# Kernel optimization log

Measured on AMD Instinct MI355X. Metric: run time of the kernel, lower is better.

Reference implementation:

```python
import jax, jax.numpy as jnp
import numpy as np

NUM_NODES = 1_000_000
MEM_DIM = 128
MSG_DIM = 128
B = 262_144


def setup_inputs() -> dict:
    key = jax.random.key(0)
    k1, k2, k3, k4, k5, k6, k7 = jax.random.split(key, 7)
    s = 1.0 / np.sqrt(MEM_DIM)
    return {
        "memory": jax.random.normal(k1, (NUM_NODES, MEM_DIM), jnp.float32) * 0.1,
        "last_update": jnp.zeros((NUM_NODES,), jnp.float32),
        "messages": jax.random.normal(k2, (B, MSG_DIM), jnp.float32),
        "timestamps": jax.random.uniform(k3, (B,), jnp.float32),
        "W_ih": jax.random.uniform(k4, (3 * MEM_DIM, MSG_DIM), jnp.float32, -s, s),
        "W_hh": jax.random.uniform(k5, (3 * MEM_DIM, MEM_DIM), jnp.float32, -s, s),
        "b_ih": jax.random.uniform(k6, (3 * MEM_DIM,), jnp.float32, -s, s),
        "b_hh": jax.random.uniform(k7, (3 * MEM_DIM,), jnp.float32, -s, s),
        "node_ids": jax.random.randint(jax.random.fold_in(key, 99), (B,), 0, NUM_NODES, jnp.int64 if jax.config.jax_enable_x64 else jnp.int32),
    }


def gru_cell(x, h, W_ih, W_hh, b_ih, b_hh):
    # torch.nn.GRUCell math
    gi = x @ W_ih.T + b_ih  # [B, 3H]
    gh = h @ W_hh.T + b_hh  # [B, 3H]
    i_r, i_z, i_n = jnp.split(gi, 3, axis=-1)
    h_r, h_z, h_n = jnp.split(gh, 3, axis=-1)
    r = jax.nn.sigmoid(i_r + h_r)
    z = jax.nn.sigmoid(i_z + h_z)
    n = jnp.tanh(i_n + r * h_n)
    return (1.0 - z) * n + z * h


def reference(memory, last_update, messages, timestamps, W_ih, W_hh, b_ih, b_hh, node_ids):
    # gather node memory rows
    h = memory[node_ids]  # [B, MEM_DIM]
    h_new = gru_cell(messages, h, W_ih, W_hh, b_ih, b_hh)
    # scatter updated state and timestamps back into persistent buffers
    memory_new = memory.at[node_ids].set(h_new)
    last_update_new = last_update.at[node_ids].set(timestamps)
    return memory_new, last_update_new
```

## Files before the change

kernel.cpp:

```cpp
#include <hip/hip_runtime.h>
#include <stdint.h>

#define NN   1000000
#define DD   128
#define BT   262144
#define TR   32
#define NT   8
#define RPB  (TR * NT)
#define GRID_GRU (BT / RPB)

typedef __attribute__((ext_vector_type(8))) short bf16x8;
typedef __attribute__((ext_vector_type(4))) float f32x4;

__device__ __forceinline__ unsigned short f2bf(float f) {
    union { float f; uint32_t u; } c; c.f = f;
    uint32_t u = c.u + 0x7FFFu + ((c.u >> 16) & 1u);
    return (unsigned short)(u >> 16);
}
__device__ __forceinline__ float bf2f(unsigned short s) {
    union { uint32_t u; float f; } c; c.u = ((uint32_t)s) << 16;
    return c.f;
}
__device__ __forceinline__ float sigmoid_f(float x) {
    return 1.0f / (1.0f + __expf(-x));
}
__device__ __forceinline__ float tanh_f(float x) {
    return 2.0f / (1.0f + __expf(-2.0f * x)) - 1.0f;
}
__device__ __forceinline__ bf16x8 cvt8(float4 a, float4 b) {
    bf16x8 v;
    v[0] = (short)f2bf(a.x); v[1] = (short)f2bf(a.y);
    v[2] = (short)f2bf(a.z); v[3] = (short)f2bf(a.w);
    v[4] = (short)f2bf(b.x); v[5] = (short)f2bf(b.y);
    v[6] = (short)f2bf(b.z); v[7] = (short)f2bf(b.w);
    return v;
}

__global__ __launch_bounds__(256) void k_winner(const int* __restrict__ node_ids,
                                                int* __restrict__ winner) {
    int i = blockIdx.x * 256 + threadIdx.x;
    if (i < BT) atomicMax(&winner[node_ids[i]], i);
}

__global__ __launch_bounds__(256) void k_copy(const float4* __restrict__ mem_in,
                                              const float* __restrict__ lu_in,
                                              const float* __restrict__ ts,
                                              const int* __restrict__ winner,
                                              float4* __restrict__ mem_out,
                                              float* __restrict__ lu_out) {
    const long NV4 = (long)NN * 32;
    const long TOTAL = NV4 + NN;
    long stride = (long)gridDim.x * 256;
    for (long i = blockIdx.x * 256L + threadIdx.x; i < TOTAL; i += stride) {
        if (i < NV4) {
            int node = (int)(i >> 5);
            if (winner[node] < 0) mem_out[i] = mem_in[i];
        } else {
            int v = (int)(i - NV4);
            int w = winner[v];
            lu_out[v] = (w >= 0) ? ts[w] : lu_in[v];
        }
    }
}

__global__ __launch_bounds__(512, 2) void k_gru(const float* __restrict__ memory,
                                                const float* __restrict__ messages,
                                                const float* __restrict__ W_ih,
                                                const float* __restrict__ W_hh,
                                                const float* __restrict__ b_ih,
                                                const float* __restrict__ b_hh,
                                                const int* __restrict__ node_ids,
                                                const int* __restrict__ winner,
                                                float* __restrict__ out_mem) {
    __shared__ unsigned short x_lds[2][TR * DD];
    __shared__ unsigned short h_lds[2][TR * DD];
    __shared__ int s_nid[RPB];
    __shared__ unsigned char s_win[RPB];

    const int tid = threadIdx.x;
    const int rowBase = blockIdx.x * RPB;

    for (int i = tid; i < RPB; i += 512) {
        int brow = rowBase + i;
        int nid = node_ids[brow];
        s_nid[i] = nid;
        s_win[i] = (winner[nid] == brow) ? 1 : 0;
    }
    __syncthreads();

    const int lane  = tid & 63;
    const int wave  = tid >> 6;
    const int l15   = lane & 15;
    const int khalf = lane >> 4;
    const int jcol  = wave * 16 + l15;

    bf16x8 wf[6][4];
#pragma unroll
    for (int g = 0; g < 3; ++g) {
#pragma unroll
        for (int ks = 0; ks < 4; ++ks) {
            const float* p = W_ih + (size_t)(g * 128 + jcol) * DD + ks * 32 + khalf * 8;
            wf[g][ks] = cvt8(*(const float4*)p, *(const float4*)(p + 4));
            const float* q = W_hh + (size_t)(g * 128 + jcol) * DD + ks * 32 + khalf * 8;
            wf[3 + g][ks] = cvt8(*(const float4*)q, *(const float4*)(q + 4));
        }
    }
    const float bir = b_ih[jcol], biz = b_ih[128 + jcol], bin = b_ih[256 + jcol];
    const float bhr = b_hh[jcol], bhz = b_hh[128 + jcol], bhn = b_hh[256 + jcol];

    const int sr  = tid >> 4;
    const int sc8 = (tid & 15) * 8;
    const int ldsOff = sr * 256 + ((sc8 * 2) ^ ((sr & 7) << 4));

    float4 px0, px1, ph0, ph1;
    {
        const float* xp = messages + (size_t)(rowBase + sr) * DD + sc8;
        px0 = ((const float4*)xp)[0]; px1 = ((const float4*)xp)[1];
        const float* hp = memory + (size_t)s_nid[sr] * DD + sc8;
        ph0 = ((const float4*)hp)[0]; ph1 = ((const float4*)hp)[1];
    }

#pragma unroll 1
    for (int t = 0; t < NT; ++t) {
        const int buf = t & 1;
        *(bf16x8*)((char*)(&x_lds[buf][0]) + ldsOff) = cvt8(px0, px1);
        *(bf16x8*)((char*)(&h_lds[buf][0]) + ldsOff) = cvt8(ph0, ph1);
        if (t + 1 < NT) {
            int r = (t + 1) * TR + sr;
            const float* xp = messages + (size_t)(rowBase + r) * DD + sc8;
            px0 = ((const float4*)xp)[0]; px1 = ((const float4*)xp)[1];
            const float* hp = memory + (size_t)s_nid[r] * DD + sc8;
            ph0 = ((const float4*)hp)[0]; ph1 = ((const float4*)hp)[1];
        }
        asm volatile("s_waitcnt lgkmcnt(0)" ::: "memory");
        __builtin_amdgcn_sched_barrier(0);
        __builtin_amdgcn_s_barrier();
        __builtin_amdgcn_sched_barrier(0);

#pragma unroll
        for (int sub = 0; sub < 2; ++sub) {
            const int arow = sub * 16 + l15;
            const char* xb = (const char*)(&x_lds[buf][0]) + arow * 256;
            const char* hb = (const char*)(&h_lds[buf][0]) + arow * 256;
            const int aswz = (arow & 7) << 4;
            bf16x8 ax[4], ah[4];
#pragma unroll
            for (int ks = 0; ks < 4; ++ks) {
                const int cb = (ks * 64 + khalf * 16) ^ aswz;
                ax[ks] = *(const bf16x8*)(xb + cb);
                ah[ks] = *(const bf16x8*)(hb + cb);
            }
            f32x4 a_ir = {0.f,0.f,0.f,0.f}, a_iz = a_ir, a_in = a_ir;
            f32x4 a_hr = a_ir, a_hz = a_ir, a_hn = a_ir;
#pragma unroll
            for (int ks = 0; ks < 4; ++ks) {
                a_ir = __builtin_amdgcn_mfma_f32_16x16x32_bf16(ax[ks], wf[0][ks], a_ir, 0, 0, 0);
                a_iz = __builtin_amdgcn_mfma_f32_16x16x32_bf16(ax[ks], wf[1][ks], a_iz, 0, 0, 0);
                a_in = __builtin_amdgcn_mfma_f32_16x16x32_bf16(ax[ks], wf[2][ks], a_in, 0, 0, 0);
                a_hr = __builtin_amdgcn_mfma_f32_16x16x32_bf16(ah[ks], wf[3][ks], a_hr, 0, 0, 0);
                a_hz = __builtin_amdgcn_mfma_f32_16x16x32_bf16(ah[ks], wf[4][ks], a_hz, 0, 0, 0);
                a_hn = __builtin_amdgcn_mfma_f32_16x16x32_bf16(ah[ks], wf[5][ks], a_hn, 0, 0, 0);
            }
#pragma unroll
            for (int q = 0; q < 4; ++q) {
                const int rl = sub * 16 + khalf * 4 + q;
                const int tr = t * TR + rl;
                float rg = sigmoid_f(a_ir[q] + bir + a_hr[q] + bhr);
                float zg = sigmoid_f(a_iz[q] + biz + a_hz[q] + bhz);
                float ng = tanh_f(a_in[q] + bin + rg * (a_hn[q] + bhn));
                unsigned short hu = *(const unsigned short*)(
                    (const char*)(&h_lds[buf][0]) + rl * 256 + ((jcol * 2) ^ ((rl & 7) << 4)));
                float h = bf2f(hu);
                float hnew = (1.0f - zg) * ng + zg * h;
                if (s_win[tr]) out_mem[(size_t)s_nid[tr] * DD + jcol] = hnew;
            }
        }
    }
}

extern "C" void kernel_launch(void* const* d_in, const int* in_sizes, int n_in,
                              void* d_out, int out_size, void* d_ws, size_t ws_size,
                              hipStream_t stream) {
    const float* memory      = (const float*)d_in[0];
    const float* last_update = (const float*)d_in[1];
    const float* messages    = (const float*)d_in[2];
    const float* timestamps  = (const float*)d_in[3];
    const float* W_ih        = (const float*)d_in[4];
    const float* W_hh        = (const float*)d_in[5];
    const float* b_ih        = (const float*)d_in[6];
    const float* b_hh        = (const float*)d_in[7];
    const int*   node_ids    = (const int*)d_in[8];

    float* out_mem = (float*)d_out;
    float* out_lu  = out_mem + (size_t)NN * DD;

    int* winner = (int*)d_ws;

    hipMemsetAsync(winner, 0xFF, (size_t)NN * sizeof(int), stream);
    k_winner<<<BT / 256, 256, 0, stream>>>(node_ids, winner);
    k_copy<<<4096, 256, 0, stream>>>((const float4*)memory, last_update, timestamps,
                                     winner, (float4*)out_mem, out_lu);
    k_gru<<<GRID_GRU, 512, 0, stream>>>(memory, messages, W_ih, W_hh, b_ih, b_hh,
                                        node_ids, winner, out_mem);
}
```

Measured before the change: 331.3 us.

## Fuse copy and GRU kernels into one launch with interleaved block roles

Merges the bulk memory/last_update copy kernel and the GRU kernel into a single launch. Every third block runs the GRU tile and the other two run a strided, 4-way unrolled copy, so the bandwidth-bound copy overlaps the MFMA-bound GRU work. It also replaces hipMemsetAsync with a small int4 init kernel and restructures the double-buffered GRU loop into two explicit register sets loaded two tiles ahead. Trade-offs: launch_bounds drops to 1 block per SM, which can reduce occupancy, and block role balance now depends on a fixed copy grid.

```diff
diff --git a/kernel.cpp b/kernel.cpp
--- a/kernel.cpp
+++ b/kernel.cpp
@@ -7,7 +7,9 @@
 #define TR   32
 #define NT   8
 #define RPB  (TR * NT)
-#define GRID_GRU (BT / RPB)
+#define GRUB (BT / RPB)
+#define CPYB 2048
+#define GRID (GRUB + CPYB)
 
 typedef __attribute__((ext_vector_type(8))) short bf16x8;
 typedef __attribute__((ext_vector_type(4))) float f32x4;
@@ -36,49 +38,62 @@
     return v;
 }
 
+__global__ __launch_bounds__(256) void k_init(int4* __restrict__ winner) {
+    int i = blockIdx.x * 256 + threadIdx.x;
+    if (i < NN / 4) winner[i] = make_int4(-1, -1, -1, -1);
+}
+
 __global__ __launch_bounds__(256) void k_winner(const int* __restrict__ node_ids,
                                                 int* __restrict__ winner) {
     int i = blockIdx.x * 256 + threadIdx.x;
     if (i < BT) atomicMax(&winner[node_ids[i]], i);
 }
 
-__global__ __launch_bounds__(256) void k_copy(const float4* __restrict__ mem_in,
-                                              const float* __restrict__ lu_in,
-                                              const float* __restrict__ ts,
-                                              const int* __restrict__ winner,
-                                              float4* __restrict__ mem_out,
-                                              float* __restrict__ lu_out) {
-    const long NV4 = (long)NN * 32;
-    const long TOTAL = NV4 + NN;
-    long stride = (long)gridDim.x * 256;
-    for (long i = blockIdx.x * 256L + threadIdx.x; i < TOTAL; i += stride) {
-        if (i < NV4) {
-            int node = (int)(i >> 5);
-            if (winner[node] < 0) mem_out[i] = mem_in[i];
-        } else {
-            int v = (int)(i - NV4);
-            int w = winner[v];
-            lu_out[v] = (w >= 0) ? ts[w] : lu_in[v];
-        }
-    }
-}
-
-__global__ __launch_bounds__(512, 2) void k_gru(const float* __restrict__ memory,
-                                                const float* __restrict__ messages,
-                                                const float* __restrict__ W_ih,
-                                                const float* __restrict__ W_hh,
-                                                const float* __restrict__ b_ih,
-                                                const float* __restrict__ b_hh,
-                                                const int* __restrict__ node_ids,
-                                                const int* __restrict__ winner,
-                                                float* __restrict__ out_mem) {
+__global__ __launch_bounds__(512, 1) void k_fused(
+        const float* __restrict__ memory,
+        const float* __restrict__ messages,
+        const float* __restrict__ W_ih,
+        const float* __restrict__ W_hh,
+        const float* __restrict__ b_ih,
+        const float* __restrict__ b_hh,
+        const int*   __restrict__ node_ids,
+        const int*   __restrict__ winner,
+        const float* __restrict__ lu_in,
+        const float* __restrict__ ts,
+        float* __restrict__ out_mem,
+        float* __restrict__ out_lu) {
     __shared__ unsigned short x_lds[2][TR * DD];
     __shared__ unsigned short h_lds[2][TR * DD];
     __shared__ int s_nid[RPB];
     __shared__ unsigned char s_win[RPB];
 
-    const int tid = threadIdx.x;
-    const int rowBase = blockIdx.x * RPB;
+    const int tid  = threadIdx.x;
+    const int role = blockIdx.x % 3;
+
+    if (role != 0) {
+        const int cid = (blockIdx.x / 3) * 2 + (role - 1);
+        const long NV4 = (long)NN * 32;
+        const long stride = (long)CPYB * 512;
+        const long base = (long)cid * 512 + tid;
+        const float4* mem4 = (const float4*)memory;
+        float4* out4 = (float4*)out_mem;
+#pragma unroll 1
+        for (long i = base; i < NV4; i += 4 * stride) {
+            long i0 = i, i1 = i + stride, i2 = i + 2 * stride, i3 = i + 3 * stride;
+            if (winner[(int)(i0 >> 5)] < 0) out4[i0] = mem4[i0];
+            if (i1 < NV4 && winner[(int)(i1 >> 5)] < 0) out4[i1] = mem4[i1];
+            if (i2 < NV4 && winner[(int)(i2 >> 5)] < 0) out4[i2] = mem4[i2];
+            if (i3 < NV4 && winner[(int)(i3 >> 5)] < 0) out4[i3] = mem4[i3];
+        }
+        if (base < NN) {
+            int w = winner[(int)base];
+            out_lu[base] = (w >= 0) ? ts[w] : lu_in[base];
+        }
+        return;
+    }
+
+    const int gid = blockIdx.x / 3;
+    const int rowBase = gid * RPB;
 
     for (int i = tid; i < RPB; i += 512) {
         int brow = rowBase + i;
@@ -112,31 +127,16 @@
     const int sc8 = (tid & 15) * 8;
     const int ldsOff = sr * 256 + ((sc8 * 2) ^ ((sr & 7) << 4));
 
-    float4 px0, px1, ph0, ph1;
-    {
-        const float* xp = messages + (size_t)(rowBase + sr) * DD + sc8;
-        px0 = ((const float4*)xp)[0]; px1 = ((const float4*)xp)[1];
-        const float* hp = memory + (size_t)s_nid[sr] * DD + sc8;
-        ph0 = ((const float4*)hp)[0]; ph1 = ((const float4*)hp)[1];
-    }
-
-#pragma unroll 1
-    for (int t = 0; t < NT; ++t) {
-        const int buf = t & 1;
-        *(bf16x8*)((char*)(&x_lds[buf][0]) + ldsOff) = cvt8(px0, px1);
-        *(bf16x8*)((char*)(&h_lds[buf][0]) + ldsOff) = cvt8(ph0, ph1);
-        if (t + 1 < NT) {
-            int r = (t + 1) * TR + sr;
-            const float* xp = messages + (size_t)(rowBase + r) * DD + sc8;
-            px0 = ((const float4*)xp)[0]; px1 = ((const float4*)xp)[1];
-            const float* hp = memory + (size_t)s_nid[r] * DD + sc8;
-            ph0 = ((const float4*)hp)[0]; ph1 = ((const float4*)hp)[1];
-        }
-        asm volatile("s_waitcnt lgkmcnt(0)" ::: "memory");
-        __builtin_amdgcn_sched_barrier(0);
-        __builtin_amdgcn_s_barrier();
-        __builtin_amdgcn_sched_barrier(0);
-
+#define GLOAD(X0, X1, H0, H1, t)                                                \
+    {                                                                           \
+        int r_ = (t) * TR + sr;                                                 \
+        const float* xp_ = messages + (size_t)(rowBase + r_) * DD + sc8;        \
+        X0 = ((const float4*)xp_)[0]; X1 = ((const float4*)xp_)[1];             \
+        const float* hp_ = memory + (size_t)s_nid[r_] * DD + sc8;               \
+        H0 = ((const float4*)hp_)[0]; H1 = ((const float4*)hp_)[1];             \
+    }
+
+    auto compute_tile = [&](int buf, int t) {
 #pragma unroll
         for (int sub = 0; sub < 2; ++sub) {
             const int arow = sub * 16 + l15;
@@ -175,7 +175,33 @@
                 if (s_win[tr]) out_mem[(size_t)s_nid[tr] * DD + jcol] = hnew;
             }
         }
-    }
+    };
+
+    float4 xA0, xA1, hA0, hA1, xB0, xB1, hB0, hB1;
+    GLOAD(xA0, xA1, hA0, hA1, 0);
+    GLOAD(xB0, xB1, hB0, hB1, 1);
+
+#pragma unroll 1
+    for (int tp = 0; tp < NT; tp += 2) {
+        *(bf16x8*)((char*)(&x_lds[0][0]) + ldsOff) = cvt8(xA0, xA1);
+        *(bf16x8*)((char*)(&h_lds[0][0]) + ldsOff) = cvt8(hA0, hA1);
+        if (tp + 2 < NT) GLOAD(xA0, xA1, hA0, hA1, tp + 2);
+        asm volatile("s_waitcnt lgkmcnt(0)" ::: "memory");
+        __builtin_amdgcn_sched_barrier(0);
+        __builtin_amdgcn_s_barrier();
+        __builtin_amdgcn_sched_barrier(0);
+        compute_tile(0, tp);
+
+        *(bf16x8*)((char*)(&x_lds[1][0]) + ldsOff) = cvt8(xB0, xB1);
+        *(bf16x8*)((char*)(&h_lds[1][0]) + ldsOff) = cvt8(hB0, hB1);
+        if (tp + 3 < NT) GLOAD(xB0, xB1, hB0, hB1, tp + 3);
+        asm volatile("s_waitcnt lgkmcnt(0)" ::: "memory");
+        __builtin_amdgcn_sched_barrier(0);
+        __builtin_amdgcn_s_barrier();
+        __builtin_amdgcn_sched_barrier(0);
+        compute_tile(1, tp + 1);
+    }
+#undef GLOAD
 }
 
 extern "C" void kernel_launch(void* const* d_in, const int* in_sizes, int n_in,
@@ -196,10 +222,9 @@
 
     int* winner = (int*)d_ws;
 
-    hipMemsetAsync(winner, 0xFF, (size_t)NN * sizeof(int), stream);
+    k_init<<<(NN / 4 + 255) / 256, 256, 0, stream>>>((int4*)winner);
     k_winner<<<BT / 256, 256, 0, stream>>>(node_ids, winner);
-    k_copy<<<4096, 256, 0, stream>>>((const float4*)memory, last_update, timestamps,
-                                     winner, (float4*)out_mem, out_lu);
-    k_gru<<<GRID_GRU, 512, 0, stream>>>(memory, messages, W_ih, W_hh, b_ih, b_hh,
-                                        node_ids, winner, out_mem);
-}
+    k_fused<<<GRID, 512, 0, stream>>>(memory, messages, W_ih, W_hh, b_ih, b_hh,
+                                      node_ids, winner, last_update, timestamps,
+                                      out_mem, out_lu);
+}
```

Result: slower. 485.4 us (+46.5%).

## Load GRU operands straight into MFMA registers, dropping LDS staging

Applied to the files above, without the earlier changes.

Removes the double-buffered LDS staging of messages and gathered memory rows. Every wave now loads its own 16-row fp32 tiles from global memory straight into MFMA operand layout and converts them to bf16 in registers, so the barriers go away. Because all 8 waves load the same rows, each gather is repeated 8 times and has to be absorbed by the cache. The fp32 h value for the blend is also read again from global, which improves precision. Separately, hipMemsetAsync is swapped for a custom init kernel and launch bounds change to 1 block per CU.

```diff
diff --git a/kernel.cpp b/kernel.cpp
--- a/kernel.cpp
+++ b/kernel.cpp
@@ -4,10 +4,8 @@
 #define NN   1000000
 #define DD   128
 #define BT   262144
-#define TR   32
-#define NT   8
-#define RPB  (TR * NT)
-#define GRID_GRU (BT / RPB)
+#define RPB  256
+#define GRUB (BT / RPB)
 
 typedef __attribute__((ext_vector_type(8))) short bf16x8;
 typedef __attribute__((ext_vector_type(4))) float f32x4;
@@ -16,10 +14,6 @@
     union { float f; uint32_t u; } c; c.f = f;
     uint32_t u = c.u + 0x7FFFu + ((c.u >> 16) & 1u);
     return (unsigned short)(u >> 16);
-}
-__device__ __forceinline__ float bf2f(unsigned short s) {
-    union { uint32_t u; float f; } c; c.u = ((uint32_t)s) << 16;
-    return c.f;
 }
 __device__ __forceinline__ float sigmoid_f(float x) {
     return 1.0f / (1.0f + __expf(-x));
@@ -34,6 +28,11 @@
     v[4] = (short)f2bf(b.x); v[5] = (short)f2bf(b.y);
     v[6] = (short)f2bf(b.z); v[7] = (short)f2bf(b.w);
     return v;
+}
+
+__global__ __launch_bounds__(256) void k_init(int4* __restrict__ winner) {
+    int i = blockIdx.x * 256 + threadIdx.x;
+    if (i < NN / 4) winner[i] = make_int4(-1, -1, -1, -1);
 }
 
 __global__ __launch_bounds__(256) void k_winner(const int* __restrict__ node_ids,
@@ -63,7 +62,7 @@
     }
 }
 
-__global__ __launch_bounds__(512, 2) void k_gru(const float* __restrict__ memory,
+__global__ __launch_bounds__(512, 1) void k_gru(const float* __restrict__ memory,
                                                 const float* __restrict__ messages,
                                                 const float* __restrict__ W_ih,
                                                 const float* __restrict__ W_hh,
@@ -72,19 +71,17 @@
                                                 const int* __restrict__ node_ids,
                                                 const int* __restrict__ winner,
                                                 float* __restrict__ out_mem) {
-    __shared__ unsigned short x_lds[2][TR * DD];
-    __shared__ unsigned short h_lds[2][TR * DD];
     __shared__ int s_nid[RPB];
     __shared__ unsigned char s_win[RPB];
 
     const int tid = threadIdx.x;
     const int rowBase = blockIdx.x * RPB;
 
-    for (int i = tid; i < RPB; i += 512) {
-        int brow = rowBase + i;
+    if (tid < RPB) {
+        int brow = rowBase + tid;
         int nid = node_ids[brow];
-        s_nid[i] = nid;
-        s_win[i] = (winner[nid] == brow) ? 1 : 0;
+        s_nid[tid] = nid;
+        s_win[tid] = (winner[nid] == brow) ? 1 : 0;
     }
     __syncthreads();
 
@@ -108,72 +105,56 @@
     const float bir = b_ih[jcol], biz = b_ih[128 + jcol], bin = b_ih[256 + jcol];
     const float bhr = b_hh[jcol], bhz = b_hh[128 + jcol], bhn = b_hh[256 + jcol];
 
-    const int sr  = tid >> 4;
-    const int sc8 = (tid & 15) * 8;
-    const int ldsOff = sr * 256 + ((sc8 * 2) ^ ((sr & 7) << 4));
+#pragma unroll 1
+    for (int t = 0; t < RPB / 16; ++t) {
+        const int rbase = t * 16;
+        const float* xp = messages + (size_t)(rowBase + rbase + l15) * DD + khalf * 8;
+        const float* hp = memory + (size_t)s_nid[rbase + l15] * DD + khalf * 8;
 
-    float4 px0, px1, ph0, ph1;
-    {
-        const float* xp = messages + (size_t)(rowBase + sr) * DD + sc8;
-        px0 = ((const float4*)xp)[0]; px1 = ((const float4*)xp)[1];
-        const float* hp = memory + (size_t)s_nid[sr] * DD + sc8;
-        ph0 = ((const float4*)hp)[0]; ph1 = ((const float4*)hp)[1];
-    }
+        float4 xf[8], hf[8];
+#pragma unroll
+        for (int ks = 0; ks < 4; ++ks) {
+            xf[2 * ks]     = *(const float4*)(xp + ks * 32);
+            xf[2 * ks + 1] = *(const float4*)(xp + ks * 32 + 4);
+            hf[2 * ks]     = *(const float4*)(hp + ks * 32);
+            hf[2 * ks + 1] = *(const float4*)(hp + ks * 32 + 4);
+        }
 
-#pragma unroll 1
-    for (int t = 0; t < NT; ++t) {
-        const int buf = t & 1;
-        *(bf16x8*)((char*)(&x_lds[buf][0]) + ldsOff) = cvt8(px0, px1);
-        *(bf16x8*)((char*)(&h_lds[buf][0]) + ldsOff) = cvt8(ph0, ph1);
-        if (t + 1 < NT) {
-            int r = (t + 1) * TR + sr;
-            const float* xp = messages + (size_t)(rowBase + r) * DD + sc8;
-            px0 = ((const float4*)xp)[0]; px1 = ((const float4*)xp)[1];
-            const float* hp = memory + (size_t)s_nid[r] * DD + sc8;
-            ph0 = ((const float4*)hp)[0]; ph1 = ((const float4*)hp)[1];
+        int enid[4]; int ewin[4]; float hq[4];
+#pragma unroll
+        for (int q = 0; q < 4; ++q) {
+            const int rl = rbase + khalf * 4 + q;
+            enid[q] = s_nid[rl];
+            ewin[q] = s_win[rl];
+            hq[q] = memory[(size_t)enid[q] * DD + jcol];
         }
-        asm volatile("s_waitcnt lgkmcnt(0)" ::: "memory");
-        __builtin_amdgcn_sched_barrier(0);
-        __builtin_amdgcn_s_barrier();
-        __builtin_amdgcn_sched_barrier(0);
+
+        bf16x8 ax[4], ah[4];
+#pragma unroll
+        for (int ks = 0; ks < 4; ++ks) {
+            ax[ks] = cvt8(xf[2 * ks], xf[2 * ks + 1]);
+            ah[ks] = cvt8(hf[2 * ks], hf[2 * ks + 1]);
+        }
+
+        f32x4 a_ir = {0.f,0.f,0.f,0.f}, a_iz = a_ir, a_in = a_ir;
+        f32x4 a_hr = a_ir, a_hz = a_ir, a_hn = a_ir;
+#pragma unroll
+        for (int ks = 0; ks < 4; ++ks) {
+            a_ir = __builtin_amdgcn_mfma_f32_16x16x32_bf16(ax[ks], wf[0][ks], a_ir, 0, 0, 0);
+            a_iz = __builtin_amdgcn_mfma_f32_16x16x32_bf16(ax[ks], wf[1][ks], a_iz, 0, 0, 0);
+            a_in = __builtin_amdgcn_mfma_f32_16x16x32_bf16(ax[ks], wf[2][ks], a_in, 0, 0, 0);
+            a_hr = __builtin_amdgcn_mfma_f32_16x16x32_bf16(ah[ks], wf[3][ks], a_hr, 0, 0, 0);
+            a_hz = __builtin_amdgcn_mfma_f32_16x16x32_bf16(ah[ks], wf[4][ks], a_hz, 0, 0, 0);
+            a_hn = __builtin_amdgcn_mfma_f32_16x16x32_bf16(ah[ks], wf[5][ks], a_hn, 0, 0, 0);
+        }
 
 #pragma unroll
-        for (int sub = 0; sub < 2; ++sub) {
-            const int arow = sub * 16 + l15;
-            const char* xb = (const char*)(&x_lds[buf][0]) + arow * 256;
-            const char* hb = (const char*)(&h_lds[buf][0]) + arow * 256;
-            const int aswz = (arow & 7) << 4;
-            bf16x8 ax[4], ah[4];
-#pragma unroll
-            for (int ks = 0; ks < 4; ++ks) {
-                const int cb = (ks * 64 + khalf * 16) ^ aswz;
-                ax[ks] = *(const bf16x8*)(xb + cb);
-                ah[ks] = *(const bf16x8*)(hb + cb);
-            }
-            f32x4 a_ir = {0.f,0.f,0.f,0.f}, a_iz = a_ir, a_in = a_ir;
-            f32x4 a_hr = a_ir, a_hz = a_ir, a_hn = a_ir;
-#pragma unroll
-            for (int ks = 0; ks < 4; ++ks) {
-                a_ir = __builtin_amdgcn_mfma_f32_16x16x32_bf16(ax[ks], wf[0][ks], a_ir, 0, 0, 0);
-                a_iz = __builtin_amdgcn_mfma_f32_16x16x32_bf16(ax[ks], wf[1][ks], a_iz, 0, 0, 0);
-                a_in = __builtin_amdgcn_mfma_f32_16x16x32_bf16(ax[ks], wf[2][ks], a_in, 0, 0, 0);
-                a_hr = __builtin_amdgcn_mfma_f32_16x16x32_bf16(ah[ks], wf[3][ks], a_hr, 0, 0, 0);
-                a_hz = __builtin_amdgcn_mfma_f32_16x16x32_bf16(ah[ks], wf[4][ks], a_hz, 0, 0, 0);
-                a_hn = __builtin_amdgcn_mfma_f32_16x16x32_bf16(ah[ks], wf[5][ks], a_hn, 0, 0, 0);
-            }
-#pragma unroll
-            for (int q = 0; q < 4; ++q) {
-                const int rl = sub * 16 + khalf * 4 + q;
-                const int tr = t * TR + rl;
-                float rg = sigmoid_f(a_ir[q] + bir + a_hr[q] + bhr);
-                float zg = sigmoid_f(a_iz[q] + biz + a_hz[q] + bhz);
-                float ng = tanh_f(a_in[q] + bin + rg * (a_hn[q] + bhn));
-                unsigned short hu = *(const unsigned short*)(
-                    (const char*)(&h_lds[buf][0]) + rl * 256 + ((jcol * 2) ^ ((rl & 7) << 4)));
-                float h = bf2f(hu);
-                float hnew = (1.0f - zg) * ng + zg * h;
-                if (s_win[tr]) out_mem[(size_t)s_nid[tr] * DD + jcol] = hnew;
-            }
+        for (int q = 0; q < 4; ++q) {
+            float rg = sigmoid_f(a_ir[q] + bir + a_hr[q] + bhr);
+            float zg = sigmoid_f(a_iz[q] + biz + a_hz[q] + bhz);
+            float ng = tanh_f(a_in[q] + bin + rg * (a_hn[q] + bhn));
+            float hnew = (1.0f - zg) * ng + zg * hq[q];
+            if (ewin[q]) out_mem[(size_t)enid[q] * DD + jcol] = hnew;
         }
     }
 }
@@ -196,10 +177,10 @@
 
     int* winner = (int*)d_ws;
 
-    hipMemsetAsync(winner, 0xFF, (size_t)NN * sizeof(int), stream);
+    k_init<<<(NN / 4 + 255) / 256, 256, 0, stream>>>((int4*)winner);
     k_winner<<<BT / 256, 256, 0, stream>>>(node_ids, winner);
     k_copy<<<4096, 256, 0, stream>>>((const float4*)memory, last_update, timestamps,
                                      winner, (float4*)out_mem, out_lu);
-    k_gru<<<GRID_GRU, 512, 0, stream>>>(memory, messages, W_ih, W_hh, b_ih, b_hh,
-                                        node_ids, winner, out_mem);
+    k_gru<<<GRUB, 512, 0, stream>>>(memory, messages, W_ih, W_hh, b_ih, b_hh,
+                                    node_ids, winner, out_mem);
 }
```

After: 486.4 us. 1.47x slower.
